# Optimization experiments

Hardware: AMD Instinct MI355X
Metric: run time of the kernel (lower is better)

Reference implementation:

```python
import jax, jax.numpy as jnp
import numpy as np

MASS, CHARGE, ALPHA, BETA = 1.0, 0.5, 0.1, 0.05
ETA = jnp.array([1.0, -1.0, -1.0, -1.0], dtype=jnp.float32)  # Minkowski metric diag


def setup_inputs() -> dict:
    key = jax.random.key(0)
    k1, k2, k3 = jax.random.split(key, 3)
    B = 262144
    y = jax.random.normal(k1, (B, 8), dtype=jnp.float32)
    W = jax.random.normal(k2, (4, 4), dtype=jnp.float32) * 0.3
    V = jax.random.normal(k3, (4, 4), dtype=jnp.float32) * 0.3
    return {"y": y, "W": W, "V": V}


def _lagrangian(z):
    # z = (x, u, A) concatenated, shape [12]
    x, u, A = z[0:4], z[4:8], z[8:12]
    kinetic = 0.5 * MASS * jnp.sum(ETA * u * u)
    coupling = CHARGE * jnp.sum(ETA * u * A)
    xu_term = ALPHA * jnp.sum((x * u) ** 2)      # makes J_xu nontrivial
    uA_term = BETA * jnp.sum(u * A) ** 2          # makes J_Au nontrivial
    return kinetic + coupling + xu_term + uA_term


def reference(y, W, V):
    def A_vec(x):  # vector potential A^mu(x), works on [4] or [B,4]
        return jnp.tanh(x @ W.T) + x @ V.T

    x = y[:, 0:4]   # [B,4] positions
    u = y[:, 4:8]   # [B,4] velocities
    A = A_vec(x)    # [B,4]
    z = jnp.concatenate([x, u, A], axis=1)  # [B,12] = (x,u,A)

    gradL = jax.vmap(jax.grad(_lagrangian))(z)      # [B,12]
    H = jax.vmap(jax.hessian(_lagrangian))(z)       # [B,12,12]

    dL_dx = gradL[:, 0:4]
    dL_dA = gradL[:, 8:12]
    J_xu = H[:, 0:4, 4:8]    # d^2L/(dx^mu du^nu)
    J_uu = H[:, 4:8, 4:8]    # d^2L/(du^mu du^nu)
    J_Au = H[:, 8:12, 4:8]   # d^2L/(dA^mu du^nu)

    # dA_dx[a, nu, i] = dA^i/dx^nu (matches tf.stack(..., axis=2) layout)
    jacA = jax.vmap(jax.jacfwd(A_vec))(x)           # [B, i, nu]
    dA_dx = jnp.transpose(jacA, (0, 2, 1))          # [B, nu, i]

    J_uu_inv = jnp.linalg.pinv(J_uu)                # [B,4,4]

    force = (dL_dx
             + jnp.einsum('ajk,ak->aj', dA_dx, dL_dA)
             - jnp.einsum('ai,aij->aj', u,
                          J_xu + jnp.einsum('ajk,akm->ajm', dA_dx, J_Au)))
    acceleration = jnp.einsum('ai,aij->aj', force, J_uu_inv)  # [B,4]
    return acceleration
```

## Files before the change

### kernel.cpp

```cpp
#include <hip/hip_runtime.h>
#include <math.h>


#define SIX_RCOND 2.86102294921875e-5
#define RCOND     4.76837158203125e-6

__device__ __forceinline__ float rcp_nr(float x) {
    float r = __builtin_amdgcn_rcpf(x);
    r = r * (2.0f - x * r);
    return r;
}

__device__ __forceinline__ void fast_tanh4(const double t[4], double th[4])
{
    const double LOG2E = 1.4426950408889634074;
    const double LN2HI = 6.93147180369123816490e-01;
    const double LN2LO = 1.90821492927058770002e-10;
    double e[4], opp[4];
    #pragma unroll
    for (int j = 0; j < 4; ++j) {
        double a  = fabs(t[j]);
        double z  = -2.0 * a;
        double zc = fmax(z, -64.0);
        double nf = rint(zc * LOG2E);
        double r  = fma(-nf, LN2HI, zc);
        r = fma(-nf, LN2LO, r);
        double p = 2.75573192239858906526e-07;
        p = fma(p, r, 2.75573192239858925110e-06);
        p = fma(p, r, 2.48015873015873015873e-05);
        p = fma(p, r, 1.98412698412698412698e-04);
        p = fma(p, r, 1.38888888888888888889e-03);
        p = fma(p, r, 8.33333333333333333333e-03);
        p = fma(p, r, 4.16666666666666666667e-02);
        p = fma(p, r, 1.66666666666666666667e-01);
        p = fma(p, r, 0.5);
        p = fma(p, r, 1.0);
        p = fma(p, r, 1.0);
        int n = (int)nf;
        double twon = __longlong_as_double(((long long)(1023 + n)) << 52);
        double ez = p * twon;
        ez = (z <= -40.0) ? 0.0 : ez;
        e[j]   = ez;
        opp[j] = 1.0 + ez;
    }
    double p01 = opp[0] * opp[1], p23 = opp[2] * opp[3];
    double rp  = 1.0 / (p01 * p23);
    double inv[4] = { opp[1] * p23 * rp, opp[0] * p23 * rp,
                      p01 * opp[3] * rp, p01 * opp[2] * rp };
    #pragma unroll
    for (int j = 0; j < 4; ++j)
        th[j] = copysign((1.0 - e[j]) * inv[j], t[j]);
}

__device__ __forceinline__ void model_terms_f64(
    const double* sW, const double* sV,
    const double x[4], const double u[4],
    double A[4], double f[4], double d[4])
{
    const double eta[4] = {1.0, -1.0, -1.0, -1.0};
    const double CHG = 0.5, ALPHA = 0.1, BETA = 0.05;
    double t[4], s[4];
    #pragma unroll
    for (int j = 0; j < 4; ++j) {
        double tj = 0.0, sj = 0.0;
        #pragma unroll
        for (int k = 0; k < 4; ++k) {
            tj = fma(sW[j*4+k], x[k], tj);
            sj = fma(sV[j*4+k], x[k], sj);
        }
        t[j] = tj; s[j] = sj;
    }
    double th[4];
    fast_tanh4(t, th);
    double G[4][4];
    #pragma unroll
    for (int j = 0; j < 4; ++j) {
        A[j] = th[j] + s[j];
        double dth = 1.0 - th[j] * th[j];
        #pragma unroll
        for (int k = 0; k < 4; ++k) G[j][k] = fma(dth, sW[j*4+k], sV[j*4+k]);
    }
    double S = 0.0;
    #pragma unroll
    for (int k = 0; k < 4; ++k) S += u[k] * A[k];
    double P[4], R[4], Q[4];
    #pragma unroll
    for (int j = 0; j < 4; ++j) {
        double p = 0.0, r = 0.0, q = 0.0;
        #pragma unroll
        for (int k = 0; k < 4; ++k) {
            p += G[k][j] * u[k];
            r += G[j][k] * u[k];
            q += G[k][j] * (CHG * eta[k]) * u[k];
        }
        P[j] = p; R[j] = r; Q[j] = q;
    }
    double T = 0.0;
    #pragma unroll
    for (int j = 0; j < 4; ++j) T += u[j] * R[j];
    #pragma unroll
    for (int j = 0; j < 4; ++j) {
        f[j] = -2.0 * ALPHA * x[j] * u[j] * u[j]
             + Q[j]
             + 2.0 * BETA * S * P[j]
             - (CHG * eta[j] + 2.0 * BETA * S) * R[j]
             - 2.0 * BETA * A[j] * T;
        d[j] = eta[j] + 2.0 * ALPHA * x[j] * x[j];
    }
}

__device__ __forceinline__ void sm_solve_f64(
    const double d[4], const double A[4], const double f[4], double acc[4])
{
    const double C2 = 0.1;
    double b[4], fd[4], den = 1.0, w = 0.0;
    #pragma unroll
    for (int j = 0; j < 4; ++j) {
        double inv = 1.0 / d[j];
        b[j]  = A[j] * inv;
        fd[j] = f[j] * inv;
        den  += C2 * A[j] * b[j];
        w    += b[j] * f[j];
    }
    double scale = C2 * w / den;
    #pragma unroll
    for (int j = 0; j < 4; ++j) acc[j] = fd[j] - b[j] * scale;
}

__device__ __forceinline__ bool criterion_f64(
    const double d[4], const double A[4])
{
    const double C2 = 0.1;
    double mind = 1e300;
    #pragma unroll
    for (int j = 0; j < 4; ++j) {
        double a = fabs(d[j]);
        mind = (a < mind) ? a : mind;
    }
    double p01 = d[0] * d[1], p23 = d[2] * d[3];
    double det = p01 * p23
        + C2 * (A[0]*A[0]*(d[1]*p23) + A[1]*A[1]*(d[0]*p23) +
                A[2]*A[2]*(p01*d[3]) + A[3]*A[3]*(p01*d[2]));
    double sumA2 = 0.0, sumA4 = 0.0, F2 = 0.0;
    #pragma unroll
    for (int j = 0; j < 4; ++j) {
        double Aj2 = A[j] * A[j];
        sumA2 += Aj2; sumA4 += Aj2 * Aj2;
        double Jjj = d[j] + C2 * Aj2;
        F2 += Jjj * Jjj;
    }
    F2 += C2 * C2 * (sumA2 * sumA2 - sumA4);
    double rowmax = 0.0;
    #pragma unroll
    for (int r = 0; r < 4; ++r) {
        double rs = 0.0;
        #pragma unroll
        for (int c = 0; c < 4; ++c) {
            double Jrc = C2 * A[r] * A[c] + ((r == c) ? d[r] : 0.0);
            rs += fabs(Jrc);
        }
        rowmax = (rs > rowmax) ? rs : rowmax;
    }
    double sig_hi2 = rowmax * rowmax;
    sig_hi2 = (F2 < sig_hi2) ? F2 : sig_hi2;
    return (fabs(det) > SIX_RCOND * sig_hi2 * sig_hi2) && (mind > 1e-3);
}

__device__ __forceinline__ void jacobi_pinv_reg(
    const double d[4], const double A[4], const double f[4], double acc[4])
{
    const double C2 = 0.1;
    double M[4][4], Vm[4][4];
    #pragma unroll
    for (int r = 0; r < 4; ++r) {
        #pragma unroll
        for (int c = 0; c < 4; ++c) {
            M[r][c] = C2 * A[r] * A[c];
            Vm[r][c] = (r == c) ? 1.0 : 0.0;
        }
        M[r][r] += d[r];
    }
    for (int sweep = 0; sweep < 8; ++sweep) {
        #pragma unroll
        for (int p = 0; p < 3; ++p) {
            #pragma unroll
            for (int q2 = p + 1; q2 < 4; ++q2) {
                double apq = M[p][q2];
                bool active = fabs(apq) > 1e-280;
                double div = active ? (2.0 * apq) : 1.0;
                double tau = (M[q2][q2] - M[p][p]) / div;
                double tt = ((tau >= 0.0) ? 1.0 : -1.0) /
                            (fabs(tau) + sqrt(1.0 + tau * tau));
                double c = 1.0 / sqrt(1.0 + tt * tt);
                double s = tt * c;
                c = active ? c : 1.0;
                s = active ? s : 0.0;
                #pragma unroll
                for (int k = 0; k < 4; ++k) {
                    double mkp = M[k][p], mkq = M[k][q2];
                    M[k][p]  = c * mkp - s * mkq;
                    M[k][q2] = s * mkp + c * mkq;
                }
                #pragma unroll
                for (int k = 0; k < 4; ++k) {
                    double mpk = M[p][k], mqk = M[q2][k];
                    M[p][k]  = c * mpk - s * mqk;
                    M[q2][k] = s * mpk + c * mqk;
                }
                #pragma unroll
                for (int k = 0; k < 4; ++k) {
                    double vkp = Vm[k][p], vkq = Vm[k][q2];
                    Vm[k][p]  = c * vkp - s * vkq;
                    Vm[k][q2] = s * vkp + c * vkq;
                }
            }
        }
    }
    double lam[4], sigmax = 0.0;
    #pragma unroll
    for (int k = 0; k < 4; ++k) {
        lam[k] = M[k][k];
        double a = fabs(lam[k]);
        sigmax = (a > sigmax) ? a : sigmax;
    }
    double cutoff = RCOND * sigmax;
    #pragma unroll
    for (int j = 0; j < 4; ++j) acc[j] = 0.0;
    #pragma unroll
    for (int e = 0; e < 4; ++e) {
        double coef = 0.0;
        #pragma unroll
        for (int k = 0; k < 4; ++k) coef += Vm[k][e] * f[k];
        coef /= lam[e];
        coef = (fabs(lam[e]) > cutoff) ? coef : 0.0;
        #pragma unroll
        for (int j = 0; j < 4; ++j) acc[j] += coef * Vm[j][e];
    }
}

__global__ __launch_bounds__(256) void fast_kernel(
    const float* __restrict__ y, const float* __restrict__ W,
    const float* __restrict__ V, float* __restrict__ out,
    unsigned int* __restrict__ cnt, int* __restrict__ list,
    unsigned int cap, int B)
{
    __shared__ float  sW[16],  sV[16];
    __shared__ double sWd[16], sVd[16];
    if (threadIdx.x < 16) {
        float w = W[threadIdx.x];
        sW[threadIdx.x]  = w;
        sWd[threadIdx.x] = (double)w;
    } else if (threadIdx.x < 32) {
        float v = V[threadIdx.x - 16];
        sV[threadIdx.x - 16]  = v;
        sVd[threadIdx.x - 16] = (double)v;
    }
    __syncthreads();

    int i = blockIdx.x * blockDim.x + threadIdx.x;
    if (i >= B) return;

    const float4* y4 = (const float4*)y;
    float4 xv = y4[2 * i];
    float4 uv = y4[2 * i + 1];
    float x[4] = {xv.x, xv.y, xv.z, xv.w};
    float u[4] = {uv.x, uv.y, uv.z, uv.w};

    const float eta[4] = {1.0f, -1.0f, -1.0f, -1.0f};
    const float CHG = 0.5f, ALPHA = 0.1f, BETA = 0.05f, C2 = 0.1f;
    const float NEG2LOG2E = -2.8853900817779268f;

    float t[4], sv[4];
    #pragma unroll
    for (int j = 0; j < 4; ++j) {
        float tj = 0.0f, sj = 0.0f;
        #pragma unroll
        for (int k = 0; k < 4; ++k) {
            tj = fmaf(sW[j*4+k], x[k], tj);
            sj = fmaf(sV[j*4+k], x[k], sj);
        }
        t[j] = tj; sv[j] = sj;
    }
    float A[4], dth[4];
    #pragma unroll
    for (int j = 0; j < 4; ++j) {
        float a  = fabsf(t[j]);
        float e  = __builtin_amdgcn_exp2f(a * NEG2LOG2E);
        float th = copysignf((1.0f - e) * rcp_nr(1.0f + e), t[j]);
        A[j]   = th + sv[j];
        dth[j] = 1.0f - th * th;
    }
    float G[4][4];
    #pragma unroll
    for (int j = 0; j < 4; ++j)
        #pragma unroll
        for (int k = 0; k < 4; ++k)
            G[j][k] = fmaf(dth[j], sW[j*4+k], sV[j*4+k]);

    float S = 0.0f;
    #pragma unroll
    for (int k = 0; k < 4; ++k) S = fmaf(u[k], A[k], S);
    float P[4], R[4], Q[4];
    #pragma unroll
    for (int j = 0; j < 4; ++j) {
        float p = 0.0f, r = 0.0f, q = 0.0f;
        #pragma unroll
        for (int k = 0; k < 4; ++k) {
            p = fmaf(G[k][j], u[k], p);
            r = fmaf(G[j][k], u[k], r);
            q = fmaf(G[k][j] * (CHG * eta[k]), u[k], q);
        }
        P[j] = p; R[j] = r; Q[j] = q;
    }
    float T = 0.0f;
    #pragma unroll
    for (int j = 0; j < 4; ++j) T = fmaf(u[j], R[j], T);
    float f[4], d[4];
    #pragma unroll
    for (int j = 0; j < 4; ++j) {
        f[j] = -2.0f * ALPHA * x[j] * u[j] * u[j]
             + Q[j]
             + 2.0f * BETA * S * P[j]
             - (CHG * eta[j] + 2.0f * BETA * S) * R[j]
             - 2.0f * BETA * A[j] * T;
        d[j] = eta[j] + 2.0f * ALPHA * x[j] * x[j];
    }

    float mind = fminf(fminf(fabsf(d[0]), fabsf(d[1])),
                       fminf(fabsf(d[2]), fabsf(d[3])));
    float p01 = d[0] * d[1], p23 = d[2] * d[3];
    float prod = p01 * p23;
    float det = prod
        + C2 * (A[0]*A[0]*(d[1]*p23) + A[1]*A[1]*(d[0]*p23) +
                A[2]*A[2]*(p01*d[3]) + A[3]*A[3]*(p01*d[2]));
    float rowmax = 0.0f;
    #pragma unroll
    for (int r = 0; r < 4; ++r) {
        float rs = 0.0f;
        #pragma unroll
        for (int c = 0; c < 4; ++c) {
            float Jrc = C2 * A[r] * A[c] + ((r == c) ? d[r] : 0.0f);
            rs += fabsf(Jrc);
        }
        rowmax = fmaxf(rs, rowmax);
    }
    float sig2 = rowmax * rowmax;
    bool safe = (fabsf(det) > sig2 * sig2 * (1.0f / 1024.0f)) && (mind > 1e-3f);

    if (safe) {
        float invprod = rcp_nr(prod);
        float invd[4] = { d[1] * p23 * invprod, d[0] * p23 * invprod,
                          p01 * d[3] * invprod, p01 * d[2] * invprod };
        float b[4], fd[4], den = 1.0f, w = 0.0f;
        #pragma unroll
        for (int j = 0; j < 4; ++j) {
            b[j]  = A[j] * invd[j];
            fd[j] = f[j] * invd[j];
            den   = fmaf(C2 * A[j], b[j], den);
            w     = fmaf(b[j], f[j], w);
        }
        float scale = (C2 * w) * rcp_nr(den);
        float4 res;
        res.x = fd[0] - b[0] * scale; res.y = fd[1] - b[1] * scale;
        res.z = fd[2] - b[2] * scale; res.w = fd[3] - b[3] * scale;
        ((float4*)out)[i] = res;
    } else {
        double xd[4] = {xv.x, xv.y, xv.z, xv.w};
        double ud[4] = {uv.x, uv.y, uv.z, uv.w};
        double Ad[4], fd64[4], dd[4];
        model_terms_f64(sWd, sVd, xd, ud, Ad, fd64, dd);
        bool safe64 = criterion_f64(dd, Ad);

        bool want = !safe64;
        unsigned long long m = __ballot(want);
        bool deferred = false;
        if (m != 0ull) {
            int lane = threadIdx.x & 63;
            int leader = __ffsll((long long)m) - 1;
            unsigned int base = 0;
            if (lane == leader)
                base = atomicAdd(cnt, (unsigned int)__popcll(m));
            base = (unsigned int)__shfl((int)base, leader);
            if (want) {
                unsigned int idx = base +
                    (unsigned int)__popcll(m & ((1ull << lane) - 1ull));
                if (idx < cap) { list[idx] = i; deferred = true; }
            }
        }
        if (!deferred) {
            double acc[4];
            sm_solve_f64(dd, Ad, fd64, acc);
            float4 res;
            res.x = (float)acc[0]; res.y = (float)acc[1];
            res.z = (float)acc[2]; res.w = (float)acc[3];
            ((float4*)out)[i] = res;
        }
    }
}

__global__ __launch_bounds__(64, 1) void slow_kernel(
    const float* __restrict__ y, const float* __restrict__ W,
    const float* __restrict__ V, float* __restrict__ out,
    const unsigned int* __restrict__ cnt, const int* __restrict__ list,
    unsigned int cap)
{
    __shared__ double sW[16], sV[16];
    if (threadIdx.x < 16)      sW[threadIdx.x]      = (double)W[threadIdx.x];
    else if (threadIdx.x < 32) sV[threadIdx.x - 16] = (double)V[threadIdx.x - 16];
    __syncthreads();

    unsigned int n = *cnt;
    if (n > cap) n = cap;
    int stride = gridDim.x * blockDim.x;
    for (unsigned int j = blockIdx.x * blockDim.x + threadIdx.x; j < n; j += stride) {
        int i = list[j];
        const float4* y4 = (const float4*)y;
        float4 xv = y4[2 * i];
        float4 uv = y4[2 * i + 1];
        double x[4] = {xv.x, xv.y, xv.z, xv.w};
        double u[4] = {uv.x, uv.y, uv.z, uv.w};
        double A[4], f[4], d[4];
        model_terms_f64(sW, sV, x, u, A, f, d);

        double acc[4];
        jacobi_pinv_reg(d, A, f, acc);

        float4 res;
        res.x = (float)acc[0]; res.y = (float)acc[1];
        res.z = (float)acc[2]; res.w = (float)acc[3];
        ((float4*)out)[i] = res;
    }
}

extern "C" void kernel_launch(void* const* d_in, const int* in_sizes, int n_in,
                              void* d_out, int out_size, void* d_ws, size_t ws_size,
                              hipStream_t stream) {
    const float* y = (const float*)d_in[0];
    const float* W = (const float*)d_in[1];
    const float* V = (const float*)d_in[2];
    float* out = (float*)d_out;
    int B = in_sizes[0] / 8;

    unsigned int* cnt = (unsigned int*)d_ws;
    int* list = (int*)((char*)d_ws + 16);
    unsigned int cap = (ws_size > 16) ? (unsigned int)((ws_size - 16) / sizeof(int)) : 0u;
    if (cap > (unsigned int)B) cap = (unsigned int)B;

    hipMemsetAsync(d_ws, 0, 16, stream);

    int block = 256;
    int grid = (B + block - 1) / block;
    fast_kernel<<<grid, block, 0, stream>>>(y, W, V, out, cnt, list, cap, B);
    slow_kernel<<<128, 64, 0, stream>>>(y, W, V, out, cnt, list, cap);
}
```

Baseline: 85.41 us.

## Fuse fast and slow paths into one kernel with per-block shared-memory compaction

Replaces the two-kernel scheme (fast kernel plus global atomic deferral list, memset, and a separate 128x64 slow kernel) with one kernel. Each block gathers its unsafe rows into a shared-memory list and then processes them densely in f64, doing the criterion check and then either the Sherman-Morrison or the Jacobi pinv solve. This removes the memset, the second launch and the serialized tail kernel, and it compacts divergent f64 work per block. The cost is that heavy Jacobi work now runs inside the main kernel, which can raise register pressure, and the launch bound of 2 may cause spills.

```diff
diff --git a/kernel.cpp b/kernel.cpp
--- a/kernel.cpp
+++ b/kernel.cpp
@@ -238,14 +238,16 @@
     }
 }
 
-__global__ __launch_bounds__(256) void fast_kernel(
+__global__ __launch_bounds__(256, 2) void fused_kernel(
     const float* __restrict__ y, const float* __restrict__ W,
-    const float* __restrict__ V, float* __restrict__ out,
-    unsigned int* __restrict__ cnt, int* __restrict__ list,
-    unsigned int cap, int B)
+    const float* __restrict__ V, float* __restrict__ out, int B)
 {
     __shared__ float  sW[16],  sV[16];
     __shared__ double sWd[16], sVd[16];
+    __shared__ int sList[256];
+    __shared__ int sCount;
+
+    if (threadIdx.x == 0) sCount = 0;
     if (threadIdx.x < 16) {
         float w = W[threadIdx.x];
         sW[threadIdx.x]  = w;
@@ -258,177 +260,140 @@
     __syncthreads();
 
     int i = blockIdx.x * blockDim.x + threadIdx.x;
-    if (i >= B) return;
-
     const float4* y4 = (const float4*)y;
-    float4 xv = y4[2 * i];
-    float4 uv = y4[2 * i + 1];
-    float x[4] = {xv.x, xv.y, xv.z, xv.w};
-    float u[4] = {uv.x, uv.y, uv.z, uv.w};
-
-    const float eta[4] = {1.0f, -1.0f, -1.0f, -1.0f};
-    const float CHG = 0.5f, ALPHA = 0.1f, BETA = 0.05f, C2 = 0.1f;
-    const float NEG2LOG2E = -2.8853900817779268f;
-
-    float t[4], sv[4];
-    #pragma unroll
-    for (int j = 0; j < 4; ++j) {
-        float tj = 0.0f, sj = 0.0f;
-        #pragma unroll
-        for (int k = 0; k < 4; ++k) {
-            tj = fmaf(sW[j*4+k], x[k], tj);
-            sj = fmaf(sV[j*4+k], x[k], sj);
-        }
-        t[j] = tj; sv[j] = sj;
-    }
-    float A[4], dth[4];
-    #pragma unroll
-    for (int j = 0; j < 4; ++j) {
-        float a  = fabsf(t[j]);
-        float e  = __builtin_amdgcn_exp2f(a * NEG2LOG2E);
-        float th = copysignf((1.0f - e) * rcp_nr(1.0f + e), t[j]);
-        A[j]   = th + sv[j];
-        dth[j] = 1.0f - th * th;
-    }
-    float G[4][4];
-    #pragma unroll
-    for (int j = 0; j < 4; ++j)
-        #pragma unroll
-        for (int k = 0; k < 4; ++k)
-            G[j][k] = fmaf(dth[j], sW[j*4+k], sV[j*4+k]);
-
-    float S = 0.0f;
-    #pragma unroll
-    for (int k = 0; k < 4; ++k) S = fmaf(u[k], A[k], S);
-    float P[4], R[4], Q[4];
-    #pragma unroll
-    for (int j = 0; j < 4; ++j) {
-        float p = 0.0f, r = 0.0f, q = 0.0f;
-        #pragma unroll
-        for (int k = 0; k < 4; ++k) {
-            p = fmaf(G[k][j], u[k], p);
-            r = fmaf(G[j][k], u[k], r);
-            q = fmaf(G[k][j] * (CHG * eta[k]), u[k], q);
-        }
-        P[j] = p; R[j] = r; Q[j] = q;
-    }
-    float T = 0.0f;
-    #pragma unroll
-    for (int j = 0; j < 4; ++j) T = fmaf(u[j], R[j], T);
-    float f[4], d[4];
-    #pragma unroll
-    for (int j = 0; j < 4; ++j) {
-        f[j] = -2.0f * ALPHA * x[j] * u[j] * u[j]
-             + Q[j]
-             + 2.0f * BETA * S * P[j]
-             - (CHG * eta[j] + 2.0f * BETA * S) * R[j]
-             - 2.0f * BETA * A[j] * T;
-        d[j] = eta[j] + 2.0f * ALPHA * x[j] * x[j];
-    }
-
-    float mind = fminf(fminf(fabsf(d[0]), fabsf(d[1])),
-                       fminf(fabsf(d[2]), fabsf(d[3])));
-    float p01 = d[0] * d[1], p23 = d[2] * d[3];
-    float prod = p01 * p23;
-    float det = prod
-        + C2 * (A[0]*A[0]*(d[1]*p23) + A[1]*A[1]*(d[0]*p23) +
-                A[2]*A[2]*(p01*d[3]) + A[3]*A[3]*(p01*d[2]));
-    float rowmax = 0.0f;
-    #pragma unroll
-    for (int r = 0; r < 4; ++r) {
-        float rs = 0.0f;
-        #pragma unroll
-        for (int c = 0; c < 4; ++c) {
-            float Jrc = C2 * A[r] * A[c] + ((r == c) ? d[r] : 0.0f);
-            rs += fabsf(Jrc);
-        }
-        rowmax = fmaxf(rs, rowmax);
-    }
-    float sig2 = rowmax * rowmax;
-    bool safe = (fabsf(det) > sig2 * sig2 * (1.0f / 1024.0f)) && (mind > 1e-3f);
-
-    if (safe) {
-        float invprod = rcp_nr(prod);
-        float invd[4] = { d[1] * p23 * invprod, d[0] * p23 * invprod,
-                          p01 * d[3] * invprod, p01 * d[2] * invprod };
-        float b[4], fd[4], den = 1.0f, w = 0.0f;
+
+    if (i < B) {
+        float4 xv = y4[2 * i];
+        float4 uv = y4[2 * i + 1];
+        float x[4] = {xv.x, xv.y, xv.z, xv.w};
+        float u[4] = {uv.x, uv.y, uv.z, uv.w};
+
+        const float eta[4] = {1.0f, -1.0f, -1.0f, -1.0f};
+        const float CHG = 0.5f, ALPHA = 0.1f, BETA = 0.05f, C2 = 0.1f;
+        const float NEG2LOG2E = -2.8853900817779268f;
+
+        float t[4], sv[4];
         #pragma unroll
         for (int j = 0; j < 4; ++j) {
-            b[j]  = A[j] * invd[j];
-            fd[j] = f[j] * invd[j];
-            den   = fmaf(C2 * A[j], b[j], den);
-            w     = fmaf(b[j], f[j], w);
-        }
-        float scale = (C2 * w) * rcp_nr(den);
-        float4 res;
-        res.x = fd[0] - b[0] * scale; res.y = fd[1] - b[1] * scale;
-        res.z = fd[2] - b[2] * scale; res.w = fd[3] - b[3] * scale;
-        ((float4*)out)[i] = res;
-    } else {
-        double xd[4] = {xv.x, xv.y, xv.z, xv.w};
-        double ud[4] = {uv.x, uv.y, uv.z, uv.w};
-        double Ad[4], fd64[4], dd[4];
-        model_terms_f64(sWd, sVd, xd, ud, Ad, fd64, dd);
-        bool safe64 = criterion_f64(dd, Ad);
-
-        bool want = !safe64;
-        unsigned long long m = __ballot(want);
-        bool deferred = false;
-        if (m != 0ull) {
-            int lane = threadIdx.x & 63;
-            int leader = __ffsll((long long)m) - 1;
-            unsigned int base = 0;
-            if (lane == leader)
-                base = atomicAdd(cnt, (unsigned int)__popcll(m));
-            base = (unsigned int)__shfl((int)base, leader);
-            if (want) {
-                unsigned int idx = base +
-                    (unsigned int)__popcll(m & ((1ull << lane) - 1ull));
-                if (idx < cap) { list[idx] = i; deferred = true; }
+            float tj = 0.0f, sj = 0.0f;
+            #pragma unroll
+            for (int k = 0; k < 4; ++k) {
+                tj = fmaf(sW[j*4+k], x[k], tj);
+                sj = fmaf(sV[j*4+k], x[k], sj);
             }
-        }
-        if (!deferred) {
+            t[j] = tj; sv[j] = sj;
+        }
+        float A[4], dth[4];
+        #pragma unroll
+        for (int j = 0; j < 4; ++j) {
+            float a  = fabsf(t[j]);
+            float e  = __builtin_amdgcn_exp2f(a * NEG2LOG2E);
+            float th = copysignf((1.0f - e) * rcp_nr(1.0f + e), t[j]);
+            A[j]   = th + sv[j];
+            dth[j] = 1.0f - th * th;
+        }
+        float G[4][4];
+        #pragma unroll
+        for (int j = 0; j < 4; ++j)
+            #pragma unroll
+            for (int k = 0; k < 4; ++k)
+                G[j][k] = fmaf(dth[j], sW[j*4+k], sV[j*4+k]);
+
+        float S = 0.0f;
+        #pragma unroll
+        for (int k = 0; k < 4; ++k) S = fmaf(u[k], A[k], S);
+        float P[4], R[4], Q[4];
+        #pragma unroll
+        for (int j = 0; j < 4; ++j) {
+            float p = 0.0f, r = 0.0f, q = 0.0f;
+            #pragma unroll
+            for (int k = 0; k < 4; ++k) {
+                p = fmaf(G[k][j], u[k], p);
+                r = fmaf(G[j][k], u[k], r);
+                q = fmaf(G[k][j] * (CHG * eta[k]), u[k], q);
+            }
+            P[j] = p; R[j] = r; Q[j] = q;
+        }
+        float T = 0.0f;
+        #pragma unroll
+        for (int j = 0; j < 4; ++j) T = fmaf(u[j], R[j], T);
+        float f[4], d[4];
+        #pragma unroll
+        for (int j = 0; j < 4; ++j) {
+            f[j] = -2.0f * ALPHA * x[j] * u[j] * u[j]
+                 + Q[j]
+                 + 2.0f * BETA * S * P[j]
+                 - (CHG * eta[j] + 2.0f * BETA * S) * R[j]
+                 - 2.0f * BETA * A[j] * T;
+            d[j] = eta[j] + 2.0f * ALPHA * x[j] * x[j];
+        }
+
+        float mind = fminf(fminf(fabsf(d[0]), fabsf(d[1])),
+                           fminf(fabsf(d[2]), fabsf(d[3])));
+        float p01 = d[0] * d[1], p23 = d[2] * d[3];
+        float prod = p01 * p23;
+        float det = prod
+            + C2 * (A[0]*A[0]*(d[1]*p23) + A[1]*A[1]*(d[0]*p23) +
+                    A[2]*A[2]*(p01*d[3]) + A[3]*A[3]*(p01*d[2]));
+        float rowmax = 0.0f;
+        #pragma unroll
+        for (int r = 0; r < 4; ++r) {
+            float rs = 0.0f;
+            #pragma unroll
+            for (int c = 0; c < 4; ++c) {
+                float Jrc = C2 * A[r] * A[c] + ((r == c) ? d[r] : 0.0f);
+                rs += fabsf(Jrc);
+            }
+            rowmax = fmaxf(rs, rowmax);
+        }
+        float sig2 = rowmax * rowmax;
+        bool safe = (fabsf(det) > sig2 * sig2 * (1.0f / 1024.0f)) && (mind > 1e-3f);
+
+        if (safe) {
+            float invprod = rcp_nr(prod);
+            float invd[4] = { d[1] * p23 * invprod, d[0] * p23 * invprod,
+                              p01 * d[3] * invprod, p01 * d[2] * invprod };
+            float b[4], fd[4], den = 1.0f, w = 0.0f;
+            #pragma unroll
+            for (int j = 0; j < 4; ++j) {
+                b[j]  = A[j] * invd[j];
+                fd[j] = f[j] * invd[j];
+                den   = fmaf(C2 * A[j], b[j], den);
+                w     = fmaf(b[j], f[j], w);
+            }
+            float scale = (C2 * w) * rcp_nr(den);
+            float4 res;
+            res.x = fd[0] - b[0] * scale; res.y = fd[1] - b[1] * scale;
+            res.z = fd[2] - b[2] * scale; res.w = fd[3] - b[3] * scale;
+            ((float4*)out)[i] = res;
+        } else {
+            int k = atomicAdd(&sCount, 1);
+            sList[k] = i;
+        }
+    }
+    __syncthreads();
+
+    int nd = sCount;
+    for (int base = 0; base < nd; base += blockDim.x) {
+        int idx = base + (int)threadIdx.x;
+        if (idx < nd) {
+            int ii = sList[idx];
+            float4 xv = y4[2 * ii];
+            float4 uv = y4[2 * ii + 1];
+            double x[4] = {xv.x, xv.y, xv.z, xv.w};
+            double u[4] = {uv.x, uv.y, uv.z, uv.w};
+            double A[4], f[4], d[4];
+            model_terms_f64(sWd, sVd, x, u, A, f, d);
+
             double acc[4];
-            sm_solve_f64(dd, Ad, fd64, acc);
+            if (criterion_f64(d, A)) sm_solve_f64(d, A, f, acc);
+            else                     jacobi_pinv_reg(d, A, f, acc);
+
             float4 res;
             res.x = (float)acc[0]; res.y = (float)acc[1];
             res.z = (float)acc[2]; res.w = (float)acc[3];
-            ((float4*)out)[i] = res;
-        }
-    }
-}
-
-__global__ __launch_bounds__(64, 1) void slow_kernel(
-    const float* __restrict__ y, const float* __restrict__ W,
-    const float* __restrict__ V, float* __restrict__ out,
-    const unsigned int* __restrict__ cnt, const int* __restrict__ list,
-    unsigned int cap)
-{
-    __shared__ double sW[16], sV[16];
-    if (threadIdx.x < 16)      sW[threadIdx.x]      = (double)W[threadIdx.x];
-    else if (threadIdx.x < 32) sV[threadIdx.x - 16] = (double)V[threadIdx.x - 16];
-    __syncthreads();
-
-    unsigned int n = *cnt;
-    if (n > cap) n = cap;
-    int stride = gridDim.x * blockDim.x;
-    for (unsigned int j = blockIdx.x * blockDim.x + threadIdx.x; j < n; j += stride) {
-        int i = list[j];
-        const float4* y4 = (const float4*)y;
-        float4 xv = y4[2 * i];
-        float4 uv = y4[2 * i + 1];
-        double x[4] = {xv.x, xv.y, xv.z, xv.w};
-        double u[4] = {uv.x, uv.y, uv.z, uv.w};
-        double A[4], f[4], d[4];
-        model_terms_f64(sW, sV, x, u, A, f, d);
-
-        double acc[4];
-        jacobi_pinv_reg(d, A, f, acc);
-
-        float4 res;
-        res.x = (float)acc[0]; res.y = (float)acc[1];
-        res.z = (float)acc[2]; res.w = (float)acc[3];
-        ((float4*)out)[i] = res;
+            ((float4*)out)[ii] = res;
+        }
     }
 }
 
@@ -441,15 +406,7 @@
     float* out = (float*)d_out;
     int B = in_sizes[0] / 8;
 
-    unsigned int* cnt = (unsigned int*)d_ws;
-    int* list = (int*)((char*)d_ws + 16);
-    unsigned int cap = (ws_size > 16) ? (unsigned int)((ws_size - 16) / sizeof(int)) : 0u;
-    if (cap > (unsigned int)B) cap = (unsigned int)B;
-
-    hipMemsetAsync(d_ws, 0, 16, stream);
-
     int block = 256;
     int grid = (B + block - 1) / block;
-    fast_kernel<<<grid, block, 0, stream>>>(y, W, V, out, cnt, list, cap, B);
-    slow_kernel<<<128, 64, 0, stream>>>(y, W, V, out, cnt, list, cap);
-}
+    fused_kernel<<<grid, block, 0, stream>>>(y, W, V, out, B);
+}
```

Result: slower. 95.61 us (+11.9%).

## Compact unsafe rows in shared memory before the fp64 fallback

Applied to the files above, without the earlier changes.

Rows that fail the fp32 safety test are now gathered into a shared-memory list with a block-level atomic. After a barrier, the first threads of the block reload those rows and run the fp64 model, criterion and solve on densely packed lanes, which removes divergence inside the fp64 branch. Launch bounds also now request two blocks per CU. The cost is an extra __syncthreads, a reload of the input for deferred rows, and a per-thread global atomic in place of the wave-aggregated one.

```diff
diff --git a/kernel.cpp b/kernel.cpp
--- a/kernel.cpp
+++ b/kernel.cpp
@@ -238,7 +238,7 @@
     }
 }
 
-__global__ __launch_bounds__(256) void fast_kernel(
+__global__ __launch_bounds__(256, 2) void fused_kernel(
     const float* __restrict__ y, const float* __restrict__ W,
     const float* __restrict__ V, float* __restrict__ out,
     unsigned int* __restrict__ cnt, int* __restrict__ list,
@@ -246,6 +246,10 @@
 {
     __shared__ float  sW[16],  sV[16];
     __shared__ double sWd[16], sVd[16];
+    __shared__ int sList[256];
+    __shared__ int sCount;
+
+    if (threadIdx.x == 0) sCount = 0;
     if (threadIdx.x < 16) {
         float w = W[threadIdx.x];
         sW[threadIdx.x]  = w;
@@ -258,142 +262,142 @@
     __syncthreads();
 
     int i = blockIdx.x * blockDim.x + threadIdx.x;
-    if (i >= B) return;
-
     const float4* y4 = (const float4*)y;
-    float4 xv = y4[2 * i];
-    float4 uv = y4[2 * i + 1];
-    float x[4] = {xv.x, xv.y, xv.z, xv.w};
-    float u[4] = {uv.x, uv.y, uv.z, uv.w};
-
-    const float eta[4] = {1.0f, -1.0f, -1.0f, -1.0f};
-    const float CHG = 0.5f, ALPHA = 0.1f, BETA = 0.05f, C2 = 0.1f;
-    const float NEG2LOG2E = -2.8853900817779268f;
-
-    float t[4], sv[4];
-    #pragma unroll
-    for (int j = 0; j < 4; ++j) {
-        float tj = 0.0f, sj = 0.0f;
-        #pragma unroll
-        for (int k = 0; k < 4; ++k) {
-            tj = fmaf(sW[j*4+k], x[k], tj);
-            sj = fmaf(sV[j*4+k], x[k], sj);
-        }
-        t[j] = tj; sv[j] = sj;
-    }
-    float A[4], dth[4];
-    #pragma unroll
-    for (int j = 0; j < 4; ++j) {
-        float a  = fabsf(t[j]);
-        float e  = __builtin_amdgcn_exp2f(a * NEG2LOG2E);
-        float th = copysignf((1.0f - e) * rcp_nr(1.0f + e), t[j]);
-        A[j]   = th + sv[j];
-        dth[j] = 1.0f - th * th;
-    }
-    float G[4][4];
-    #pragma unroll
-    for (int j = 0; j < 4; ++j)
-        #pragma unroll
-        for (int k = 0; k < 4; ++k)
-            G[j][k] = fmaf(dth[j], sW[j*4+k], sV[j*4+k]);
-
-    float S = 0.0f;
-    #pragma unroll
-    for (int k = 0; k < 4; ++k) S = fmaf(u[k], A[k], S);
-    float P[4], R[4], Q[4];
-    #pragma unroll
-    for (int j = 0; j < 4; ++j) {
-        float p = 0.0f, r = 0.0f, q = 0.0f;
-        #pragma unroll
-        for (int k = 0; k < 4; ++k) {
-            p = fmaf(G[k][j], u[k], p);
-            r = fmaf(G[j][k], u[k], r);
-            q = fmaf(G[k][j] * (CHG * eta[k]), u[k], q);
-        }
-        P[j] = p; R[j] = r; Q[j] = q;
-    }
-    float T = 0.0f;
-    #pragma unroll
-    for (int j = 0; j < 4; ++j) T = fmaf(u[j], R[j], T);
-    float f[4], d[4];
-    #pragma unroll
-    for (int j = 0; j < 4; ++j) {
-        f[j] = -2.0f * ALPHA * x[j] * u[j] * u[j]
-             + Q[j]
-             + 2.0f * BETA * S * P[j]
-             - (CHG * eta[j] + 2.0f * BETA * S) * R[j]
-             - 2.0f * BETA * A[j] * T;
-        d[j] = eta[j] + 2.0f * ALPHA * x[j] * x[j];
-    }
-
-    float mind = fminf(fminf(fabsf(d[0]), fabsf(d[1])),
-                       fminf(fabsf(d[2]), fabsf(d[3])));
-    float p01 = d[0] * d[1], p23 = d[2] * d[3];
-    float prod = p01 * p23;
-    float det = prod
-        + C2 * (A[0]*A[0]*(d[1]*p23) + A[1]*A[1]*(d[0]*p23) +
-                A[2]*A[2]*(p01*d[3]) + A[3]*A[3]*(p01*d[2]));
-    float rowmax = 0.0f;
-    #pragma unroll
-    for (int r = 0; r < 4; ++r) {
-        float rs = 0.0f;
-        #pragma unroll
-        for (int c = 0; c < 4; ++c) {
-            float Jrc = C2 * A[r] * A[c] + ((r == c) ? d[r] : 0.0f);
-            rs += fabsf(Jrc);
-        }
-        rowmax = fmaxf(rs, rowmax);
-    }
-    float sig2 = rowmax * rowmax;
-    bool safe = (fabsf(det) > sig2 * sig2 * (1.0f / 1024.0f)) && (mind > 1e-3f);
-
-    if (safe) {
-        float invprod = rcp_nr(prod);
-        float invd[4] = { d[1] * p23 * invprod, d[0] * p23 * invprod,
-                          p01 * d[3] * invprod, p01 * d[2] * invprod };
-        float b[4], fd[4], den = 1.0f, w = 0.0f;
+
+    if (i < B) {
+        float4 xv = y4[2 * i];
+        float4 uv = y4[2 * i + 1];
+        float x[4] = {xv.x, xv.y, xv.z, xv.w};
+        float u[4] = {uv.x, uv.y, uv.z, uv.w};
+
+        const float eta[4] = {1.0f, -1.0f, -1.0f, -1.0f};
+        const float CHG = 0.5f, ALPHA = 0.1f, BETA = 0.05f, C2 = 0.1f;
+        const float NEG2LOG2E = -2.8853900817779268f;
+
+        float t[4], sv[4];
         #pragma unroll
         for (int j = 0; j < 4; ++j) {
-            b[j]  = A[j] * invd[j];
-            fd[j] = f[j] * invd[j];
-            den   = fmaf(C2 * A[j], b[j], den);
-            w     = fmaf(b[j], f[j], w);
-        }
-        float scale = (C2 * w) * rcp_nr(den);
-        float4 res;
-        res.x = fd[0] - b[0] * scale; res.y = fd[1] - b[1] * scale;
-        res.z = fd[2] - b[2] * scale; res.w = fd[3] - b[3] * scale;
-        ((float4*)out)[i] = res;
-    } else {
-        double xd[4] = {xv.x, xv.y, xv.z, xv.w};
-        double ud[4] = {uv.x, uv.y, uv.z, uv.w};
-        double Ad[4], fd64[4], dd[4];
-        model_terms_f64(sWd, sVd, xd, ud, Ad, fd64, dd);
-        bool safe64 = criterion_f64(dd, Ad);
-
-        bool want = !safe64;
-        unsigned long long m = __ballot(want);
+            float tj = 0.0f, sj = 0.0f;
+            #pragma unroll
+            for (int k = 0; k < 4; ++k) {
+                tj = fmaf(sW[j*4+k], x[k], tj);
+                sj = fmaf(sV[j*4+k], x[k], sj);
+            }
+            t[j] = tj; sv[j] = sj;
+        }
+        float A[4], dth[4];
+        #pragma unroll
+        for (int j = 0; j < 4; ++j) {
+            float a  = fabsf(t[j]);
+            float e  = __builtin_amdgcn_exp2f(a * NEG2LOG2E);
+            float th = copysignf((1.0f - e) * rcp_nr(1.0f + e), t[j]);
+            A[j]   = th + sv[j];
+            dth[j] = 1.0f - th * th;
+        }
+        float G[4][4];
+        #pragma unroll
+        for (int j = 0; j < 4; ++j)
+            #pragma unroll
+            for (int k = 0; k < 4; ++k)
+                G[j][k] = fmaf(dth[j], sW[j*4+k], sV[j*4+k]);
+
+        float S = 0.0f;
+        #pragma unroll
+        for (int k = 0; k < 4; ++k) S = fmaf(u[k], A[k], S);
+        float P[4], R[4], Q[4];
+        #pragma unroll
+        for (int j = 0; j < 4; ++j) {
+            float p = 0.0f, r = 0.0f, q = 0.0f;
+            #pragma unroll
+            for (int k = 0; k < 4; ++k) {
+                p = fmaf(G[k][j], u[k], p);
+                r = fmaf(G[j][k], u[k], r);
+                q = fmaf(G[k][j] * (CHG * eta[k]), u[k], q);
+            }
+            P[j] = p; R[j] = r; Q[j] = q;
+        }
+        float T = 0.0f;
+        #pragma unroll
+        for (int j = 0; j < 4; ++j) T = fmaf(u[j], R[j], T);
+        float f[4], d[4];
+        #pragma unroll
+        for (int j = 0; j < 4; ++j) {
+            f[j] = -2.0f * ALPHA * x[j] * u[j] * u[j]
+                 + Q[j]
+                 + 2.0f * BETA * S * P[j]
+                 - (CHG * eta[j] + 2.0f * BETA * S) * R[j]
+                 - 2.0f * BETA * A[j] * T;
+            d[j] = eta[j] + 2.0f * ALPHA * x[j] * x[j];
+        }
+
+        float mind = fminf(fminf(fabsf(d[0]), fabsf(d[1])),
+                           fminf(fabsf(d[2]), fabsf(d[3])));
+        float p01 = d[0] * d[1], p23 = d[2] * d[3];
+        float prod = p01 * p23;
+        float det = prod
+            + C2 * (A[0]*A[0]*(d[1]*p23) + A[1]*A[1]*(d[0]*p23) +
+                    A[2]*A[2]*(p01*d[3]) + A[3]*A[3]*(p01*d[2]));
+        float rowmax = 0.0f;
+        #pragma unroll
+        for (int r = 0; r < 4; ++r) {
+            float rs = 0.0f;
+            #pragma unroll
+            for (int c = 0; c < 4; ++c) {
+                float Jrc = C2 * A[r] * A[c] + ((r == c) ? d[r] : 0.0f);
+                rs += fabsf(Jrc);
+            }
+            rowmax = fmaxf(rs, rowmax);
+        }
+        float sig2 = rowmax * rowmax;
+        bool safe = (fabsf(det) > sig2 * sig2 * (1.0f / 1024.0f)) && (mind > 1e-3f);
+
+        if (safe) {
+            float invprod = rcp_nr(prod);
+            float invd[4] = { d[1] * p23 * invprod, d[0] * p23 * invprod,
+                              p01 * d[3] * invprod, p01 * d[2] * invprod };
+            float b[4], fd[4], den = 1.0f, w = 0.0f;
+            #pragma unroll
+            for (int j = 0; j < 4; ++j) {
+                b[j]  = A[j] * invd[j];
+                fd[j] = f[j] * invd[j];
+                den   = fmaf(C2 * A[j], b[j], den);
+                w     = fmaf(b[j], f[j], w);
+            }
+            float scale = (C2 * w) * rcp_nr(den);
+            float4 res;
+            res.x = fd[0] - b[0] * scale; res.y = fd[1] - b[1] * scale;
+            res.z = fd[2] - b[2] * scale; res.w = fd[3] - b[3] * scale;
+            ((float4*)out)[i] = res;
+        } else {
+            int k = atomicAdd(&sCount, 1);
+            sList[k] = i;
+        }
+    }
+    __syncthreads();
+
+    int nd = sCount;
+    if ((int)threadIdx.x < nd) {
+        int ii = sList[threadIdx.x];
+        float4 xv = y4[2 * ii];
+        float4 uv = y4[2 * ii + 1];
+        double x[4] = {xv.x, xv.y, xv.z, xv.w};
+        double u[4] = {uv.x, uv.y, uv.z, uv.w};
+        double A[4], f[4], d[4];
+        model_terms_f64(sWd, sVd, x, u, A, f, d);
+
+        bool safe64 = criterion_f64(d, A);
         bool deferred = false;
-        if (m != 0ull) {
-            int lane = threadIdx.x & 63;
-            int leader = __ffsll((long long)m) - 1;
-            unsigned int base = 0;
-            if (lane == leader)
-                base = atomicAdd(cnt, (unsigned int)__popcll(m));
-            base = (unsigned int)__shfl((int)base, leader);
-            if (want) {
-                unsigned int idx = base +
-                    (unsigned int)__popcll(m & ((1ull << lane) - 1ull));
-                if (idx < cap) { list[idx] = i; deferred = true; }
-            }
+        if (!safe64) {
+            unsigned int idx = atomicAdd(cnt, 1u);
+            if (idx < cap) { list[idx] = ii; deferred = true; }
         }
         if (!deferred) {
             double acc[4];
-            sm_solve_f64(dd, Ad, fd64, acc);
+            sm_solve_f64(d, A, f, acc);
             float4 res;
             res.x = (float)acc[0]; res.y = (float)acc[1];
             res.z = (float)acc[2]; res.w = (float)acc[3];
-            ((float4*)out)[i] = res;
+            ((float4*)out)[ii] = res;
         }
     }
 }
@@ -450,6 +454,6 @@
 
     int block = 256;
     int grid = (B + block - 1) / block;
-    fast_kernel<<<grid, block, 0, stream>>>(y, W, V, out, cnt, list, cap, B);
+    fused_kernel<<<grid, block, 0, stream>>>(y, W, V, out, cnt, list, cap, B);
     slow_kernel<<<128, 64, 0, stream>>>(y, W, V, out, cnt, list, cap);
 }
```

Result: no change. 85.68 us (+0.3%).

## Split fp64 fallback into separate mid kernel with three-stage compaction

Applied to the files above, without the earlier changes.

The fp64 recheck path moves out of the fast kernel into a new mid kernel that reads a compacted list of flagged rows. Rows that still fail go into a second list that stores their precomputed A, f and d, so the slow Jacobi kernel no longer recomputes the model terms. The fast kernel drops its shared-memory staging of W and V and reads them straight from global memory, restructures the G/P/Q/R accumulation, and the Jacobi sweep count falls from 8 to 6. This removes fp64 divergence and register pressure from the fast kernel, at the cost of an extra launch, a serial dependency chain and fewer Jacobi sweeps, which may reduce accuracy on hard cases.

```diff
diff --git a/kernel.cpp b/kernel.cpp
--- a/kernel.cpp
+++ b/kernel.cpp
@@ -53,7 +53,7 @@
 }
 
 __device__ __forceinline__ void model_terms_f64(
-    const double* sW, const double* sV,
+    const float* __restrict__ W, const float* __restrict__ V,
     const double x[4], const double u[4],
     double A[4], double f[4], double d[4])
 {
@@ -65,8 +65,8 @@
         double tj = 0.0, sj = 0.0;
         #pragma unroll
         for (int k = 0; k < 4; ++k) {
-            tj = fma(sW[j*4+k], x[k], tj);
-            sj = fma(sV[j*4+k], x[k], sj);
+            tj = fma((double)W[j*4+k], x[k], tj);
+            sj = fma((double)V[j*4+k], x[k], sj);
         }
         t[j] = tj; s[j] = sj;
     }
@@ -78,7 +78,8 @@
         A[j] = th[j] + s[j];
         double dth = 1.0 - th[j] * th[j];
         #pragma unroll
-        for (int k = 0; k < 4; ++k) G[j][k] = fma(dth, sW[j*4+k], sV[j*4+k]);
+        for (int k = 0; k < 4; ++k)
+            G[j][k] = fma(dth, (double)W[j*4+k], (double)V[j*4+k]);
     }
     double S = 0.0;
     #pragma unroll
@@ -180,7 +181,7 @@
         }
         M[r][r] += d[r];
     }
-    for (int sweep = 0; sweep < 8; ++sweep) {
+    for (int sweep = 0; sweep < 6; ++sweep) {
         #pragma unroll
         for (int p = 0; p < 3; ++p) {
             #pragma unroll
@@ -241,22 +242,9 @@
 __global__ __launch_bounds__(256) void fast_kernel(
     const float* __restrict__ y, const float* __restrict__ W,
     const float* __restrict__ V, float* __restrict__ out,
-    unsigned int* __restrict__ cnt, int* __restrict__ list,
-    unsigned int cap, int B)
-{
-    __shared__ float  sW[16],  sV[16];
-    __shared__ double sWd[16], sVd[16];
-    if (threadIdx.x < 16) {
-        float w = W[threadIdx.x];
-        sW[threadIdx.x]  = w;
-        sWd[threadIdx.x] = (double)w;
-    } else if (threadIdx.x < 32) {
-        float v = V[threadIdx.x - 16];
-        sV[threadIdx.x - 16]  = v;
-        sVd[threadIdx.x - 16] = (double)v;
-    }
-    __syncthreads();
-
+    unsigned int* __restrict__ cnt1, int* __restrict__ list1,
+    unsigned int cap1, int B)
+{
     int i = blockIdx.x * blockDim.x + threadIdx.x;
     if (i >= B) return;
 
@@ -276,8 +264,8 @@
         float tj = 0.0f, sj = 0.0f;
         #pragma unroll
         for (int k = 0; k < 4; ++k) {
-            tj = fmaf(sW[j*4+k], x[k], tj);
-            sj = fmaf(sV[j*4+k], x[k], sj);
+            tj = fmaf(W[j*4+k], x[k], tj);
+            sj = fmaf(V[j*4+k], x[k], sj);
         }
         t[j] = tj; sv[j] = sj;
     }
@@ -290,31 +278,28 @@
         A[j]   = th + sv[j];
         dth[j] = 1.0f - th * th;
     }
-    float G[4][4];
-    #pragma unroll
-    for (int j = 0; j < 4; ++j)
-        #pragma unroll
-        for (int k = 0; k < 4; ++k)
-            G[j][k] = fmaf(dth[j], sW[j*4+k], sV[j*4+k]);
-
-    float S = 0.0f;
-    #pragma unroll
-    for (int k = 0; k < 4; ++k) S = fmaf(u[k], A[k], S);
-    float P[4], R[4], Q[4];
-    #pragma unroll
-    for (int j = 0; j < 4; ++j) {
-        float p = 0.0f, r = 0.0f, q = 0.0f;
-        #pragma unroll
-        for (int k = 0; k < 4; ++k) {
-            p = fmaf(G[k][j], u[k], p);
-            r = fmaf(G[j][k], u[k], r);
-            q = fmaf(G[k][j] * (CHG * eta[k]), u[k], q);
-        }
-        P[j] = p; R[j] = r; Q[j] = q;
-    }
-    float T = 0.0f;
-    #pragma unroll
-    for (int j = 0; j < 4; ++j) T = fmaf(u[j], R[j], T);
+
+    float P[4] = {0,0,0,0}, Q[4] = {0,0,0,0}, R[4];
+    #pragma unroll
+    for (int k = 0; k < 4; ++k) {
+        float g[4];
+        #pragma unroll
+        for (int j = 0; j < 4; ++j) g[j] = fmaf(dth[k], W[k*4+j], V[k*4+j]);
+        float r = 0.0f;
+        #pragma unroll
+        for (int j = 0; j < 4; ++j) r = fmaf(g[j], u[j], r);
+        R[k] = r;
+        float cu  = u[k];
+        float cue = (CHG * eta[k]) * u[k];
+        #pragma unroll
+        for (int j = 0; j < 4; ++j) {
+            P[j] = fmaf(g[j], cu,  P[j]);
+            Q[j] = fmaf(g[j], cue, Q[j]);
+        }
+    }
+    float S = 0.0f, T = 0.0f;
+    #pragma unroll
+    for (int k = 0; k < 4; ++k) { S = fmaf(u[k], A[k], S); T = fmaf(u[k], R[k], T); }
     float f[4], d[4];
     #pragma unroll
     for (int j = 0; j < 4; ++j) {
@@ -347,7 +332,23 @@
     float sig2 = rowmax * rowmax;
     bool safe = (fabsf(det) > sig2 * sig2 * (1.0f / 1024.0f)) && (mind > 1e-3f);
 
-    if (safe) {
+    bool want = !safe;
+    unsigned long long m = __ballot(want);
+    bool deferred = false;
+    if (m != 0ull) {
+        int lane = threadIdx.x & 63;
+        int leader = __ffsll((long long)m) - 1;
+        unsigned int base = 0;
+        if (lane == leader)
+            base = atomicAdd(cnt1, (unsigned int)__popcll(m));
+        base = (unsigned int)__shfl((int)base, leader);
+        if (want) {
+            unsigned int idx = base +
+                (unsigned int)__popcll(m & ((1ull << lane) - 1ull));
+            if (idx < cap1) { list1[idx] = i; deferred = true; }
+        }
+    }
+    if (!deferred) {
         float invprod = rcp_nr(prod);
         float invd[4] = { d[1] * p23 * invprod, d[0] * p23 * invprod,
                           p01 * d[3] * invprod, p01 * d[2] * invprod };
@@ -364,14 +365,39 @@
         res.x = fd[0] - b[0] * scale; res.y = fd[1] - b[1] * scale;
         res.z = fd[2] - b[2] * scale; res.w = fd[3] - b[3] * scale;
         ((float4*)out)[i] = res;
-    } else {
-        double xd[4] = {xv.x, xv.y, xv.z, xv.w};
-        double ud[4] = {uv.x, uv.y, uv.z, uv.w};
-        double Ad[4], fd64[4], dd[4];
-        model_terms_f64(sWd, sVd, xd, ud, Ad, fd64, dd);
-        bool safe64 = criterion_f64(dd, Ad);
-
-        bool want = !safe64;
+    }
+}
+
+__global__ __launch_bounds__(64, 1) void mid_kernel(
+    const float* __restrict__ y, const float* __restrict__ W,
+    const float* __restrict__ V, float* __restrict__ out,
+    const unsigned int* __restrict__ cnt1, const int* __restrict__ list1,
+    unsigned int cap1,
+    unsigned int* __restrict__ cnt2, double* __restrict__ data2,
+    int* __restrict__ idx2, unsigned int cap2)
+{
+    unsigned int n = *cnt1;
+    if (n > cap1) n = cap1;
+    unsigned int stride = gridDim.x * blockDim.x;
+    for (unsigned int j = blockIdx.x * blockDim.x + threadIdx.x; ; j += stride) {
+        bool live = (j < n);
+        if (__ballot(live) == 0ull) break;
+
+        int ii = 0;
+        double A[4], f[4], d[4];
+        bool safe64 = true;
+        if (live) {
+            ii = list1[j];
+            const float4* y4 = (const float4*)y;
+            float4 xv = y4[2 * ii];
+            float4 uv = y4[2 * ii + 1];
+            double x[4] = {xv.x, xv.y, xv.z, xv.w};
+            double u[4] = {uv.x, uv.y, uv.z, uv.w};
+            model_terms_f64(W, V, x, u, A, f, d);
+            safe64 = criterion_f64(d, A);
+        }
+
+        bool want = live && !safe64;
         unsigned long long m = __ballot(want);
         bool deferred = false;
         if (m != 0ull) {
@@ -379,48 +405,54 @@
             int leader = __ffsll((long long)m) - 1;
             unsigned int base = 0;
             if (lane == leader)
-                base = atomicAdd(cnt, (unsigned int)__popcll(m));
+                base = atomicAdd(cnt2, (unsigned int)__popcll(m));
             base = (unsigned int)__shfl((int)base, leader);
             if (want) {
                 unsigned int idx = base +
                     (unsigned int)__popcll(m & ((1ull << lane) - 1ull));
-                if (idx < cap) { list[idx] = i; deferred = true; }
+                if (idx < cap2) {
+                    double* rec = data2 + (size_t)idx * 12;
+                    #pragma unroll
+                    for (int k = 0; k < 4; ++k) rec[k]     = A[k];
+                    #pragma unroll
+                    for (int k = 0; k < 4; ++k) rec[4 + k] = f[k];
+                    #pragma unroll
+                    for (int k = 0; k < 4; ++k) rec[8 + k] = d[k];
+                    idx2[idx] = ii;
+                    deferred = true;
+                }
             }
         }
-        if (!deferred) {
+        if (live && !deferred) {
             double acc[4];
-            sm_solve_f64(dd, Ad, fd64, acc);
+            sm_solve_f64(d, A, f, acc);
             float4 res;
             res.x = (float)acc[0]; res.y = (float)acc[1];
             res.z = (float)acc[2]; res.w = (float)acc[3];
-            ((float4*)out)[i] = res;
-        }
+            ((float4*)out)[ii] = res;
+        }
+        if (j + stride >= n && j >= n) break;
     }
 }
 
 __global__ __launch_bounds__(64, 1) void slow_kernel(
-    const float* __restrict__ y, const float* __restrict__ W,
-    const float* __restrict__ V, float* __restrict__ out,
-    const unsigned int* __restrict__ cnt, const int* __restrict__ list,
-    unsigned int cap)
-{
-    __shared__ double sW[16], sV[16];
-    if (threadIdx.x < 16)      sW[threadIdx.x]      = (double)W[threadIdx.x];
-    else if (threadIdx.x < 32) sV[threadIdx.x - 16] = (double)V[threadIdx.x - 16];
-    __syncthreads();
-
-    unsigned int n = *cnt;
-    if (n > cap) n = cap;
-    int stride = gridDim.x * blockDim.x;
+    float* __restrict__ out,
+    const unsigned int* __restrict__ cnt2, const double* __restrict__ data2,
+    const int* __restrict__ idx2, unsigned int cap2)
+{
+    unsigned int n = *cnt2;
+    if (n > cap2) n = cap2;
+    unsigned int stride = gridDim.x * blockDim.x;
     for (unsigned int j = blockIdx.x * blockDim.x + threadIdx.x; j < n; j += stride) {
-        int i = list[j];
-        const float4* y4 = (const float4*)y;
-        float4 xv = y4[2 * i];
-        float4 uv = y4[2 * i + 1];
-        double x[4] = {xv.x, xv.y, xv.z, xv.w};
-        double u[4] = {uv.x, uv.y, uv.z, uv.w};
+        const double* rec = data2 + (size_t)j * 12;
         double A[4], f[4], d[4];
-        model_terms_f64(sW, sV, x, u, A, f, d);
+        #pragma unroll
+        for (int k = 0; k < 4; ++k) A[k] = rec[k];
+        #pragma unroll
+        for (int k = 0; k < 4; ++k) f[k] = rec[4 + k];
+        #pragma unroll
+        for (int k = 0; k < 4; ++k) d[k] = rec[8 + k];
+        int i = idx2[j];
 
         double acc[4];
         jacobi_pinv_reg(d, A, f, acc);
@@ -441,15 +473,30 @@
     float* out = (float*)d_out;
     int B = in_sizes[0] / 8;
 
-    unsigned int* cnt = (unsigned int*)d_ws;
-    int* list = (int*)((char*)d_ws + 16);
-    unsigned int cap = (ws_size > 16) ? (unsigned int)((ws_size - 16) / sizeof(int)) : 0u;
-    if (cap > (unsigned int)B) cap = (unsigned int)B;
+    unsigned int* cnt1 = (unsigned int*)d_ws;
+    unsigned int* cnt2 = cnt1 + 1;
+    unsigned int cap1 = 0, cap2 = 0;
+    if (ws_size > 16) {
+        size_t avail = ws_size - 16;
+        cap1 = (unsigned int)B;
+        if ((size_t)cap1 * 4 > avail / 2) cap1 = (unsigned int)(avail / 8);
+        size_t rem = avail - (size_t)cap1 * 4;
+        cap2 = (unsigned int)(rem / (12 * sizeof(double) + sizeof(int)));
+        if (cap2 > (unsigned int)B) cap2 = (unsigned int)B;
+        if (cap2 > 65536u) cap2 = 65536u;
+    }
+    int* list1 = (int*)((char*)d_ws + 16);
+    char* p2 = (char*)d_ws + 16 + (size_t)cap1 * 4;
+    p2 = (char*)(((size_t)p2 + 7) & ~(size_t)7);
+    double* data2 = (double*)p2;
+    int* idx2 = (int*)(p2 + (size_t)cap2 * 12 * sizeof(double));
 
     hipMemsetAsync(d_ws, 0, 16, stream);
 
     int block = 256;
     int grid = (B + block - 1) / block;
-    fast_kernel<<<grid, block, 0, stream>>>(y, W, V, out, cnt, list, cap, B);
-    slow_kernel<<<128, 64, 0, stream>>>(y, W, V, out, cnt, list, cap);
-}
+    fast_kernel<<<grid, block, 0, stream>>>(y, W, V, out, cnt1, list1, cap1, B);
+    mid_kernel<<<128, 64, 0, stream>>>(y, W, V, out, cnt1, list1, cap1,
+                                       cnt2, data2, idx2, cap2);
+    slow_kernel<<<64, 64, 0, stream>>>(out, cnt2, data2, idx2, cap2);
+}
```

Measured after the change: 91.17 us. 6.7% more time.
